# Kernel optimization log

Hardware: AMD Instinct MI355X
Metric: run time of the kernel (lower is better)

## Reference

```python
import jax, jax.numpy as jnp
import numpy as np
from jax import lax

NEG = -1e30  # finite stand-in for -inf (stable under logaddexp and grads)
B, T, C, L = 256, 512, 256, 128  # batch, time, num_classes (blank = C-1), max label len


def setup_inputs() -> dict:
    key = jax.random.key(0)
    k1, k2, k3 = jax.random.split(key, 3)
    logits = jax.random.normal(k1, (B, T, C), dtype=jnp.float32)
    y_pred = jax.nn.softmax(logits, axis=-1)            # keras expects softmax probs
    y_true = jax.random.randint(k2, (B, L), 0, C - 1).astype(jnp.int32)  # exclude blank
    input_length = jnp.full((B, 1), T, dtype=jnp.int32)
    label_length = jax.random.randint(k3, (B, 1), L // 2, L + 1).astype(jnp.int32)
    return {"y_true": y_true, "y_pred": y_pred,
            "input_length": input_length, "label_length": label_length}


def _ctc_batch_cost(y_true, y_pred, input_length, label_length):
    Bb, Tt, Cc = y_pred.shape
    Ll = y_true.shape[1]
    S = 2 * Ll + 1
    blank = Cc - 1
    # keras ctc_batch_cost: logits = log(y_pred + eps); tf.nn.ctc_loss then applies
    # log_softmax internally (softmax(log p) == p for normalized p, up to eps).
    logp = jax.nn.log_softmax(jnp.log(y_pred + 1e-7), axis=-1)        # [B,T,C]

    # extended label sequence: blank, l1, blank, l2, ..., blank  -> [B,S]
    ext = jnp.full((Bb, S), blank, dtype=jnp.int32)
    ext = ext.at[:, 1::2].set(y_true.astype(jnp.int32))
    same_prev = jnp.concatenate(
        [jnp.ones((Bb, 2), bool), ext[:, 2:] == ext[:, :-2]], axis=1)
    can_skip = (ext != blank) & (~same_prev)                           # [B,S]

    # emission log-prob per extended position: emit[b,t,s] = logp[b,t,ext[b,s]]
    emit = jnp.take_along_axis(
        logp, jnp.broadcast_to(ext[:, None, :], (Bb, Tt, S)), axis=2)  # [B,T,S]

    alpha0 = jnp.full((Bb, S), NEG, dtype=logp.dtype)
    alpha0 = alpha0.at[:, 0].set(emit[:, 0, 0]).at[:, 1].set(emit[:, 0, 1])
    inlen = input_length[:, 0]

    def step(alpha, xs):
        emit_t, t = xs                                    # [B,S], scalar
        s1 = jnp.concatenate([jnp.full((Bb, 1), NEG, alpha.dtype), alpha[:, :-1]], 1)
        s2 = jnp.concatenate([jnp.full((Bb, 2), NEG, alpha.dtype), alpha[:, :-2]], 1)
        s2 = jnp.where(can_skip, s2, NEG)
        new = jnp.logaddexp(jnp.logaddexp(alpha, s1), s2) + emit_t
        alpha = jnp.where((t < inlen)[:, None], new, alpha)  # freeze past input_length
        return alpha, None

    xs = (emit[:, 1:].transpose(1, 0, 2), jnp.arange(1, Tt))
    alphaT, _ = lax.scan(step, alpha0, xs)

    lab = jnp.clip(label_length[:, 0], 1, Ll)
    idx = jnp.stack([2 * lab - 1, 2 * lab], axis=1)                    # [B,2]
    ends = jnp.take_along_axis(alphaT, idx, axis=1)
    loss = -jnp.logaddexp(ends[:, 0], ends[:, 1])                      # [B]
    return loss[:, None]                                               # [B,1] like keras


def reference(y_true, y_pred, input_length, label_length):
    return _ctc_batch_cost(y_true, y_pred, input_length, label_length)
```

## Files before the change

kernel.cpp:

```cpp
#include <hip/hip_runtime.h>
#include <math.h>

#define NEGVF (-1e30f)
#define CTC_T 512
#define CTC_C 256
#define CTC_L 128
#define BLANKC (CTC_C - 1)

#if __has_builtin(__builtin_amdgcn_exp2f)
__device__ __forceinline__ float fexp2(float x) { return __builtin_amdgcn_exp2f(x); }
#else
__device__ __forceinline__ float fexp2(float x) { return exp2f(x); }
#endif
#if __has_builtin(__builtin_amdgcn_logf)
__device__ __forceinline__ float flog2(float x) { return __builtin_amdgcn_logf(x); }
#else
__device__ __forceinline__ float flog2(float x) { return log2f(x); }
#endif

__device__ __forceinline__ float lae2(float a, float b) {
    float m = fmaxf(a, b);
    float n = fminf(a, b);
    return m + flog2(1.0f + fexp2(n - m));
}

__device__ __forceinline__ float dpp_shr1_f(float x) {
    return __int_as_float(__builtin_amdgcn_update_dpp(
        0, __float_as_int(x), 0x138, 0xF, 0xF, true));
}
__device__ __forceinline__ int dpp_shr1_i(int x) {
    return __builtin_amdgcn_update_dpp(0, x, 0x138, 0xF, 0xF, true);
}

__global__ __launch_bounds__(64) void ctc_fwd_kernel(
    const int* __restrict__ y_true,
    const float* __restrict__ y_pred,
    const int* __restrict__ in_len,
    const int* __restrict__ lab_len,
    float* __restrict__ out)
{
    __shared__ float sh[2 * CTC_L + 1];

    const int b = blockIdx.x;
    const int k = threadIdx.x;

    const float* __restrict__ ybase = y_pred + (size_t)b * CTC_T * CTC_C;
    const uint64_t ybase_u = (uint64_t)(uintptr_t)ybase;
    const int* __restrict__ yt = y_true + (size_t)b * CTC_L;

    const int l0 = yt[2 * k];
    const int l1 = yt[2 * k + 1];
    const int lm1 = __shfl_up(l1, 1);
    const float sk1f = ((k > 0) && (l0 != lm1) && (l0 != BLANKC)) ? 1.0f : 0.0f;
    const float sk3f = ((l1 != l0) && (l1 != BLANKC)) ? 1.0f : 0.0f;

    int inl = in_len[b];
    if (inl > CTC_T) inl = CTC_T;
    const int nsteps = inl - 1;

    float pb0 = ybase[BLANKC];
    float p00 = ybase[l0];
    float a0 = (k == 0) ? pb0 : 0.0f;
    float a1 = (k == 0) ? p00 : 0.0f;
    float a2 = 0.0f, a3 = 0.0f, a4 = 0.0f;
    int   E  = 0;
    float pm3raw = 0.0f;

    int v_ofb = BLANKC * 4;
    int v_of0 = l0 * 4;
    int v_of1 = l1 * 4;

    float bufb[3][8], buf0[3][8], buf1[3][8];

    uint64_t baseA = ybase_u + 1024;
    uint64_t baseB = baseA + 4096;

#define LOAD1(dst, voff, rb) \
    asm volatile("global_load_dword %0, %1, %2" \
                 : "=v"(dst) : "v"(voff), "s"(rb) : "memory")
#define LOAD1O(dst, voff, rb, OFF) \
    asm volatile("global_load_dword %0, %1, %2 offset:" OFF \
                 : "=v"(dst) : "v"(voff), "s"(rb) : "memory")

#define STGF(stg, r, base, OFF) { \
    LOAD1O(bufb[stg][r], v_ofb, base, OFF); \
    LOAD1O(buf0[stg][r], v_of0, base, OFF); \
    LOAD1O(buf1[stg][r], v_of1, base, OFF); }
#define STAGE_FAST(stg) { \
    STGF(stg, 0, baseA, "0")    STGF(stg, 1, baseA, "1024") \
    STGF(stg, 2, baseA, "2048") STGF(stg, 3, baseA, "3072") \
    STGF(stg, 4, baseB, "0")    STGF(stg, 5, baseB, "1024") \
    STGF(stg, 6, baseB, "2048") STGF(stg, 7, baseB, "3072") }

#define STGS(stg, r, t0) { \
    int rr = (t0) + (r); if (rr > nsteps) rr = nsteps; \
    uint64_t rb = ybase_u + (uint64_t)rr * (CTC_C * 4); \
    LOAD1(bufb[stg][r], v_ofb, rb); \
    LOAD1(buf0[stg][r], v_of0, rb); \
    LOAD1(buf1[stg][r], v_of1, rb); }
#define STAGE_SLOW(stg, t0) { \
    STGS(stg, 0, t0) STGS(stg, 1, t0) STGS(stg, 2, t0) STGS(stg, 3, t0) \
    STGS(stg, 4, t0) STGS(stg, 5, t0) STGS(stg, 6, t0) STGS(stg, 7, t0) }

#define LSTEP(cur, r, dX) { \
    float eb = bufb[cur][r]; \
    float e0 = buf0[cur][r]; \
    float e1 = buf1[cur][r]; \
    float pmu = ldexpf(pm3raw, dX); \
    float a3n = fmaf(sk3f, a1, a3 + a2) * e1; \
    pm3raw = dpp_shr1_f(a3n); \
    float a0n = (a0 + pmu) * eb; \
    float a1n = fmaf(sk1f, pmu, a1 + a0) * e0; \
    float a2n = (a2 + a1) * eb; \
    a4 = (a4 + a3) * eb; \
    a0 = a0n; a1 = a1n; a2 = a2n; a3 = a3n; \
}

#define BODY(cur, stg) { \
    int t0s = tbase + 16; \
    if (t0s + 7 <= nsteps) { STAGE_FAST(stg); } \
    else                   { STAGE_SLOW(stg, t0s); } \
    baseA += 8192; baseB += 8192; \
    int EnbOld = dpp_shr1_i(E);   \
    float m = fmaxf(fmaxf(fmaxf(a0, a1), fmaxf(a2, a3)), a4); \
    float mm = m * 0x1p64f;                  \
    int exm = (__float_as_int(mm) >> 23) & 0xff; \
    bool dead = (exm == 0);                  \
    int dd = dead ? 0 : (191 - exm);         \
    a0 = ldexpf(a0, dd); a1 = ldexpf(a1, dd); a2 = ldexpf(a2, dd); \
    a3 = ldexpf(a3, dd); a4 = ldexpf(a4, dd); \
    E -= dd; \
    int E0 = __builtin_amdgcn_readfirstlane(E);  \
    E = dead ? E0 : E; \
    int Enb = dpp_shr1_i(E); \
    int dnb  = Enb - E;      \
    int dadj = EnbOld - E;   \
    asm volatile("s_waitcnt vmcnt(48)" ::: "memory"); \
    __builtin_amdgcn_sched_barrier(0); \
    if (tbase + 7 <= nsteps) { \
        LSTEP(cur, 0, dadj) LSTEP(cur, 1, dnb) LSTEP(cur, 2, dnb) \
        LSTEP(cur, 3, dnb)  LSTEP(cur, 4, dnb) LSTEP(cur, 5, dnb) \
        LSTEP(cur, 6, dnb)  LSTEP(cur, 7, dnb) \
    } else { \
        int rem = nsteps - tbase; \
        LSTEP(cur, 0, dadj) \
        if (rem > 0) { LSTEP(cur, 1, dnb) } \
        if (rem > 1) { LSTEP(cur, 2, dnb) } \
        if (rem > 2) { LSTEP(cur, 3, dnb) } \
        if (rem > 3) { LSTEP(cur, 4, dnb) } \
        if (rem > 4) { LSTEP(cur, 5, dnb) } \
        if (rem > 5) { LSTEP(cur, 6, dnb) } \
        if (rem > 6) { LSTEP(cur, 7, dnb) } \
    } \
}

    const int nb2 = (nsteps > 0) ? ((nsteps + 7) >> 3) : 0;
    int tbase = 1;

    if (nb2 >= 1) {
        __builtin_amdgcn_sched_barrier(0);
        if (8 <= nsteps)  { STAGE_FAST(0); } else { STAGE_SLOW(0, 1); }
        baseA += 8192; baseB += 8192;
        if (16 <= nsteps) { STAGE_FAST(1); } else { STAGE_SLOW(1, 9); }
        baseA += 8192; baseB += 8192;
        int j = 0;
        for (;;) {
            BODY(0, 2); tbase += 8; if (++j >= nb2) break;
            BODY(1, 0); tbase += 8; if (++j >= nb2) break;
            BODY(2, 1); tbase += 8; if (++j >= nb2) break;
        }
    }

    float l0v = fmaxf(flog2(a0) + (float)E, NEGVF);
    float l1v = fmaxf(flog2(a1) + (float)E, NEGVF);
    float l2v = fmaxf(flog2(a2) + (float)E, NEGVF);
    float l3v = fmaxf(flog2(a3) + (float)E, NEGVF);
    float l4v = fmaxf(flog2(a4) + (float)E, NEGVF);

    sh[4 * k + 0] = l0v;
    sh[4 * k + 1] = l1v;
    sh[4 * k + 2] = l2v;
    sh[4 * k + 3] = l3v;
    if (k == 63) sh[256] = l4v;
    __syncthreads();
    if (k == 0) {
        int ll = lab_len[b];
        if (ll < 1) ll = 1;
        if (ll > CTC_L) ll = CTC_L;
        float ea = sh[2 * ll - 1];
        float eb = sh[2 * ll];
        int cnt = 1 + (nsteps > 0 ? nsteps : 0);
        const float LSE2 = flog2(1.0f + (float)CTC_C * 1e-7f);
        out[b] = -0.69314718055994530942f * (lae2(ea, eb) - (float)cnt * LSE2);
    }
#undef LOAD1
#undef LOAD1O
#undef STGF
#undef STAGE_FAST
#undef STGS
#undef STAGE_SLOW
#undef LSTEP
#undef BODY
}

extern "C" void kernel_launch(void* const* d_in, const int* in_sizes, int n_in,
                              void* d_out, int out_size, void* d_ws, size_t ws_size,
                              hipStream_t stream) {
    (void)n_in; (void)d_ws; (void)ws_size; (void)out_size;
    const int* y_true = (const int*)d_in[0];
    const float* y_pred = (const float*)d_in[1];
    const int* in_len = (const int*)d_in[2];
    const int* lab_len = (const int*)d_in[3];
    float* out = (float*)d_out;
    const int B = in_sizes[2];
    ctc_fwd_kernel<<<B, 64, 0, stream>>>(y_true, y_pred, in_len, lab_len, out);
}
```

Measured before the change: 33.76 us.

## Load full rows with dwordx4 and gather emissions through LDS ring buffer

Instead of three scattered dword gathers per thread per timestep (blank, l0, l1), each thread loads a coalesced 16-byte chunk of the probability row. The row is written to a 4-slot LDS ring, and the three needed values are read back from it two steps ahead. This cuts the number of memory instructions and avoids uncoalesced gathers. The cost is an LDS round trip per step on the serial recurrence path, no barrier despite cross-lane LDS dependencies (relies on single-wave execution), and retuned vmcnt waits.

Result: slower. 43.45 us (+28.7%).

```diff
diff --git a/kernel.cpp b/kernel.cpp
--- a/kernel.cpp
+++ b/kernel.cpp
@@ -6,6 +6,8 @@
 #define CTC_C 256
 #define CTC_L 128
 #define BLANKC (CTC_C - 1)
+
+typedef float f4 __attribute__((ext_vector_type(4)));
 
 #if __has_builtin(__builtin_amdgcn_exp2f)
 __device__ __forceinline__ float fexp2(float x) { return __builtin_amdgcn_exp2f(x); }
@@ -39,6 +41,7 @@
     const int* __restrict__ lab_len,
     float* __restrict__ out)
 {
+    __shared__ float rowbufF[4][CTC_C];
     __shared__ float sh[2 * CTC_L + 1];
 
     const int b = blockIdx.x;
@@ -66,91 +69,99 @@
     int   E  = 0;
     float pm3raw = 0.0f;
 
-    int v_ofb = BLANKC * 4;
-    int v_of0 = l0 * 4;
-    int v_of1 = l1 * 4;
-
-    float bufb[3][8], buf0[3][8], buf1[3][8];
+    const int v_off4 = k << 4;
+
+    f4 bufrow[3][8];
 
     uint64_t baseA = ybase_u + 1024;
     uint64_t baseB = baseA + 4096;
 
-#define LOAD1(dst, voff, rb) \
-    asm volatile("global_load_dword %0, %1, %2" \
-                 : "=v"(dst) : "v"(voff), "s"(rb) : "memory")
-#define LOAD1O(dst, voff, rb, OFF) \
-    asm volatile("global_load_dword %0, %1, %2 offset:" OFF \
-                 : "=v"(dst) : "v"(voff), "s"(rb) : "memory")
-
-#define STGF(stg, r, base, OFF) { \
-    LOAD1O(bufb[stg][r], v_ofb, base, OFF); \
-    LOAD1O(buf0[stg][r], v_of0, base, OFF); \
-    LOAD1O(buf1[stg][r], v_of1, base, OFF); }
+#define LOAD4(dst, rb) \
+    asm volatile("global_load_dwordx4 %0, %1, %2" \
+                 : "=v"(dst) : "v"(v_off4), "s"(rb) : "memory")
+#define LOAD4O(dst, rb, OFF) \
+    asm volatile("global_load_dwordx4 %0, %1, %2 offset:" OFF \
+                 : "=v"(dst) : "v"(v_off4), "s"(rb) : "memory")
+
 #define STAGE_FAST(stg) { \
-    STGF(stg, 0, baseA, "0")    STGF(stg, 1, baseA, "1024") \
-    STGF(stg, 2, baseA, "2048") STGF(stg, 3, baseA, "3072") \
-    STGF(stg, 4, baseB, "0")    STGF(stg, 5, baseB, "1024") \
-    STGF(stg, 6, baseB, "2048") STGF(stg, 7, baseB, "3072") }
+    LOAD4O(bufrow[stg][0], baseA, "0");    LOAD4O(bufrow[stg][1], baseA, "1024"); \
+    LOAD4O(bufrow[stg][2], baseA, "2048"); LOAD4O(bufrow[stg][3], baseA, "3072"); \
+    LOAD4O(bufrow[stg][4], baseB, "0");    LOAD4O(bufrow[stg][5], baseB, "1024"); \
+    LOAD4O(bufrow[stg][6], baseB, "2048"); LOAD4O(bufrow[stg][7], baseB, "3072"); }
 
 #define STGS(stg, r, t0) { \
     int rr = (t0) + (r); if (rr > nsteps) rr = nsteps; \
     uint64_t rb = ybase_u + (uint64_t)rr * (CTC_C * 4); \
-    LOAD1(bufb[stg][r], v_ofb, rb); \
-    LOAD1(buf0[stg][r], v_of0, rb); \
-    LOAD1(buf1[stg][r], v_of1, rb); }
+    LOAD4(bufrow[stg][r], rb); }
 #define STAGE_SLOW(stg, t0) { \
     STGS(stg, 0, t0) STGS(stg, 1, t0) STGS(stg, 2, t0) STGS(stg, 3, t0) \
     STGS(stg, 4, t0) STGS(stg, 5, t0) STGS(stg, 6, t0) STGS(stg, 7, t0) }
 
-#define LSTEP(cur, r, dX) { \
-    float eb = bufb[cur][r]; \
-    float e0 = buf0[cur][r]; \
-    float e1 = buf1[cur][r]; \
+    float pbC, p0C, p1C, pbM, p0M, p1M, pbN, p0N, p1N;
+
+#define PREPX(srcf4, S, pbX, p0X, p1X) { \
+    ((f4*)rowbufF[S])[k] = (srcf4); \
+    pbX = rowbufF[S][BLANKC]; \
+    p0X = rowbufF[S][l0]; \
+    p1X = rowbufF[S][l1]; }
+
+#define SSTEP(dX, srcf4, S) { \
+    PREPX(srcf4, S, pbN, p0N, p1N); \
     float pmu = ldexpf(pm3raw, dX); \
-    float a3n = fmaf(sk3f, a1, a3 + a2) * e1; \
+    float a3n = fmaf(sk3f, a1, a3 + a2) * p1C; \
     pm3raw = dpp_shr1_f(a3n); \
-    float a0n = (a0 + pmu) * eb; \
-    float a1n = fmaf(sk1f, pmu, a1 + a0) * e0; \
-    float a2n = (a2 + a1) * eb; \
-    a4 = (a4 + a3) * eb; \
+    float a0n = (a0 + pmu) * pbC; \
+    float a1n = fmaf(sk1f, pmu, a1 + a0) * p0C; \
+    float a2n = (a2 + a1) * pbC; \
+    a4 = (a4 + a3) * pbC; \
     a0 = a0n; a1 = a1n; a2 = a2n; a3 = a3n; \
-}
-
-#define BODY(cur, stg) { \
+    pbC = pbM; p0C = p0M; p1C = p1M; \
+    pbM = pbN; p0M = p0N; p1M = p1N; }
+
+#define BODY(cur, nxt, stg) { \
     int t0s = tbase + 16; \
     if (t0s + 7 <= nsteps) { STAGE_FAST(stg); } \
     else                   { STAGE_SLOW(stg, t0s); } \
     baseA += 8192; baseB += 8192; \
-    int EnbOld = dpp_shr1_i(E);   \
+    int EnbOld = dpp_shr1_i(E); \
     float m = fmaxf(fmaxf(fmaxf(a0, a1), fmaxf(a2, a3)), a4); \
-    float mm = m * 0x1p64f;                  \
+    float mm = m * 0x1p64f; \
     int exm = (__float_as_int(mm) >> 23) & 0xff; \
-    bool dead = (exm == 0);                  \
-    int dd = dead ? 0 : (191 - exm);         \
+    bool dead = (exm == 0); \
+    int dd = dead ? 0 : (191 - exm); \
     a0 = ldexpf(a0, dd); a1 = ldexpf(a1, dd); a2 = ldexpf(a2, dd); \
     a3 = ldexpf(a3, dd); a4 = ldexpf(a4, dd); \
     E -= dd; \
-    int E0 = __builtin_amdgcn_readfirstlane(E);  \
+    int E0 = __builtin_amdgcn_readfirstlane(E); \
     E = dead ? E0 : E; \
     int Enb = dpp_shr1_i(E); \
-    int dnb  = Enb - E;      \
-    int dadj = EnbOld - E;   \
-    asm volatile("s_waitcnt vmcnt(48)" ::: "memory"); \
+    int dnb  = Enb - E; \
+    int dadj = EnbOld - E; \
+    asm volatile("s_waitcnt vmcnt(16)" ::: "memory"); \
     __builtin_amdgcn_sched_barrier(0); \
     if (tbase + 7 <= nsteps) { \
-        LSTEP(cur, 0, dadj) LSTEP(cur, 1, dnb) LSTEP(cur, 2, dnb) \
-        LSTEP(cur, 3, dnb)  LSTEP(cur, 4, dnb) LSTEP(cur, 5, dnb) \
-        LSTEP(cur, 6, dnb)  LSTEP(cur, 7, dnb) \
+        SSTEP(dadj, bufrow[cur][2], 3) \
+        SSTEP(dnb,  bufrow[cur][3], 0) \
+        SSTEP(dnb,  bufrow[cur][4], 1) \
+        SSTEP(dnb,  bufrow[cur][5], 2) \
+        SSTEP(dnb,  bufrow[cur][6], 3) \
+        SSTEP(dnb,  bufrow[cur][7], 0) \
+        asm volatile("s_waitcnt vmcnt(15)" ::: "memory"); \
+        SSTEP(dnb,  bufrow[nxt][0], 1) \
+        asm volatile("s_waitcnt vmcnt(14)" ::: "memory"); \
+        SSTEP(dnb,  bufrow[nxt][1], 2) \
     } else { \
         int rem = nsteps - tbase; \
-        LSTEP(cur, 0, dadj) \
-        if (rem > 0) { LSTEP(cur, 1, dnb) } \
-        if (rem > 1) { LSTEP(cur, 2, dnb) } \
-        if (rem > 2) { LSTEP(cur, 3, dnb) } \
-        if (rem > 3) { LSTEP(cur, 4, dnb) } \
-        if (rem > 4) { LSTEP(cur, 5, dnb) } \
-        if (rem > 5) { LSTEP(cur, 6, dnb) } \
-        if (rem > 6) { LSTEP(cur, 7, dnb) } \
+        SSTEP(dadj, bufrow[cur][2], 3) \
+        if (rem > 0) { SSTEP(dnb, bufrow[cur][3], 0) } \
+        if (rem > 1) { SSTEP(dnb, bufrow[cur][4], 1) } \
+        if (rem > 2) { SSTEP(dnb, bufrow[cur][5], 2) } \
+        if (rem > 3) { SSTEP(dnb, bufrow[cur][6], 3) } \
+        if (rem > 4) { SSTEP(dnb, bufrow[cur][7], 0) } \
+        if (rem > 5) { asm volatile("s_waitcnt vmcnt(15)" ::: "memory"); \
+                       SSTEP(dnb, bufrow[nxt][0], 1) } \
+        if (rem > 6) { asm volatile("s_waitcnt vmcnt(14)" ::: "memory"); \
+                       SSTEP(dnb, bufrow[nxt][1], 2) } \
     } \
 }
 
@@ -163,11 +174,15 @@
         baseA += 8192; baseB += 8192;
         if (16 <= nsteps) { STAGE_FAST(1); } else { STAGE_SLOW(1, 9); }
         baseA += 8192; baseB += 8192;
+        asm volatile("s_waitcnt vmcnt(14)" ::: "memory");
+        __builtin_amdgcn_sched_barrier(0);
+        PREPX(bufrow[0][0], 1, pbC, p0C, p1C);
+        PREPX(bufrow[0][1], 2, pbM, p0M, p1M);
         int j = 0;
         for (;;) {
-            BODY(0, 2); tbase += 8; if (++j >= nb2) break;
-            BODY(1, 0); tbase += 8; if (++j >= nb2) break;
-            BODY(2, 1); tbase += 8; if (++j >= nb2) break;
+            BODY(0, 1, 2); tbase += 8; if (++j >= nb2) break;
+            BODY(1, 2, 0); tbase += 8; if (++j >= nb2) break;
+            BODY(2, 0, 1); tbase += 8; if (++j >= nb2) break;
         }
     }
 
@@ -193,13 +208,13 @@
         const float LSE2 = flog2(1.0f + (float)CTC_C * 1e-7f);
         out[b] = -0.69314718055994530942f * (lae2(ea, eb) - (float)cnt * LSE2);
     }
-#undef LOAD1
-#undef LOAD1O
-#undef STGF
+#undef LOAD4
+#undef LOAD4O
 #undef STAGE_FAST
 #undef STGS
 #undef STAGE_SLOW
-#undef LSTEP
+#undef PREPX
+#undef SSTEP
 #undef BODY
 }
 
```
